# Optimization experiments

Hardware: AMD Instinct MI355X
Metric: run time of the kernel (lower is better)

The kernel has to match this reference:

```python
import jax, jax.numpy as jnp
import numpy as np

NEG_SLOPE = 0.2

def _gat_conv(x, src, dst, W, att_src, att_dst, bias, num_nodes):
    # x: [N, Fin], W: [H*C, Fin], att_*: [H, C], bias: [H*C]
    H, C = att_src.shape
    xh = (x @ W.T).reshape(num_nodes, H, C)            # [N,H,C]
    a_s = jnp.einsum('nhc,hc->nh', xh, att_src)         # [N,H]
    a_d = jnp.einsum('nhc,hc->nh', xh, att_dst)
    e = jax.nn.leaky_relu(a_s[src] + a_d[dst], NEG_SLOPE)  # [E,H]
    # segment softmax over destination node per head
    m = jax.ops.segment_max(e, dst, num_segments=num_nodes)      # [N,H]
    ex = jnp.exp(e - m[dst])
    s = jax.ops.segment_sum(ex, dst, num_segments=num_nodes)     # [N,H]
    alpha = ex / (s[dst] + 1e-16)                                # [E,H]
    msg = xh[src] * alpha[:, :, None]                            # [E,H,C]
    out = jax.ops.segment_sum(msg, dst, num_segments=num_nodes)  # [N,H,C]
    return out.reshape(num_nodes, H * C) + bias


def setup_inputs() -> dict:
    key = jax.random.key(0)
    ks = jax.random.split(key, 16)
    N, E, Fin, Hd, H1, G = 50000, 800000, 128, 128, 4, 128
    x = jax.random.normal(ks[0], (N, Fin), dtype=jnp.float32)
    edge_index = jax.random.randint(ks[1], (2, E), 0, N, dtype=jnp.int64)
    batch = jnp.sort(jax.random.randint(ks[2], (N,), 0, G, dtype=jnp.int64))
    sc1 = 1.0 / np.sqrt(Fin)
    sc2 = 1.0 / np.sqrt(Hd * H1)
    sch = 1.0 / np.sqrt(Hd)
    return {
        'x': x, 'edge_index': edge_index, 'batch': batch,
        'W1': jax.random.normal(ks[3], (Hd * H1, Fin), dtype=jnp.float32) * sc1,
        'as1': jax.random.normal(ks[4], (H1, Hd), dtype=jnp.float32) * 0.1,
        'ad1': jax.random.normal(ks[5], (H1, Hd), dtype=jnp.float32) * 0.1,
        'b1': jnp.zeros((Hd * H1,), dtype=jnp.float32),
        'W2': jax.random.normal(ks[6], (Hd, Hd * H1), dtype=jnp.float32) * sc2,
        'as2': jax.random.normal(ks[7], (1, Hd), dtype=jnp.float32) * 0.1,
        'ad2': jax.random.normal(ks[8], (1, Hd), dtype=jnp.float32) * 0.1,
        'b2': jnp.zeros((Hd,), dtype=jnp.float32),
        'Wh1': jax.random.normal(ks[9], (Hd, Hd), dtype=jnp.float32) * sch,
        'bh1': jnp.zeros((Hd,), dtype=jnp.float32),
        'Wh2': jax.random.normal(ks[10], (1, Hd), dtype=jnp.float32) * sch,
        'bh2': jnp.zeros((1,), dtype=jnp.float32),
    }


def reference(x, edge_index, batch, W1, as1, ad1, b1, W2, as2, ad2, b2, Wh1, bh1, Wh2, bh2):
    N = x.shape[0]
    G = 128  # num graphs
    # add self loops (PyG GATConv default)
    loops = jnp.arange(N, dtype=edge_index.dtype)
    src = jnp.concatenate([edge_index[0], loops])
    dst = jnp.concatenate([edge_index[1], loops])
    h = _gat_conv(x, src, dst, W1, as1, ad1, b1, N)   # [N, 512]
    h = jax.nn.elu(h)
    h = _gat_conv(h, src, dst, W2, as2, ad2, b2, N)   # [N, 128]
    h = jax.nn.elu(h)
    # global mean pool over batch
    sums = jax.ops.segment_sum(h, batch, num_segments=G)
    cnts = jax.ops.segment_sum(jnp.ones((N,), dtype=h.dtype), batch, num_segments=G)
    pooled = sums / jnp.maximum(cnts, 1.0)[:, None]   # [G, 128]
    z = jax.nn.relu(pooled @ Wh1.T + bh1)
    out = z @ Wh2.T + bh2                             # [G, 1]
    return out.reshape(-1)
```

## Files before the change

kernel.cpp:

```cpp
#include <hip/hip_runtime.h>
#include <cstdint>
#include <cstddef>

#define NEG_SLOPE 0.2f

typedef _Float16 f16x8 __attribute__((ext_vector_type(8)));
typedef _Float16 f16x2 __attribute__((ext_vector_type(2)));
typedef float    f32x4 __attribute__((ext_vector_type(4)));

__device__ __forceinline__ float leaky(float x){ return x > 0.f ? x : NEG_SLOPE * x; }
__device__ __forceinline__ float elu(float x){ return x > 0.f ? x : __expf(x) - 1.f; }

__global__ void k_wcvt(const float* __restrict__ src, _Float16* __restrict__ hi,
                       _Float16* __restrict__ lo, int n)
{
    int i = blockIdx.x * 256 + threadIdx.x;
    if (i >= n) return;
    float v = src[i];
    _Float16 h = (_Float16)v;
    hi[i] = h;
    lo[i] = (_Float16)(v - (float)h);
}

#define LSG 40
#define CP  136
template<bool FUSE_BIAS_ELU>
__global__ __launch_bounds__(256, 2) void k_gemm_h(
    const _Float16* __restrict__ A, const _Float16* __restrict__ Bh,
    const _Float16* __restrict__ Bl, const float* __restrict__ bias,
    _Float16* __restrict__ C,
    int M, int K, int lda, int ldb, int ldc,
    long aZ, long bZ, long cZ, long biasZ)
{
    __shared__ __align__(16) _Float16 smem[128 * CP];
    _Float16* As  = smem;
    _Float16* Bhs = smem + 128 * LSG;
    _Float16* Bls = smem + 256 * LSG;

    const _Float16* Ab  = A  + (size_t)blockIdx.z * aZ;
    const _Float16* Bhb = Bh + (size_t)blockIdx.z * bZ;
    const _Float16* Blb = Bl + (size_t)blockIdx.z * bZ;
    _Float16* Cb = C + (size_t)blockIdx.z * cZ;

    const int tid = threadIdx.x;
    const int wave = tid >> 6, lane = tid & 63;
    const int wm = wave >> 1, wn = wave & 1;
    const int quad = lane >> 4, l16 = lane & 15;
    const int m0 = blockIdx.x * 128;

    f32x4 acc[4][4] = {};

    for (int k0 = 0; k0 < K; k0 += 32) {
        #pragma unroll
        for (int q = 0; q < 2; ++q) {
            int idx = tid + q * 256;
            int row = idx >> 2, kq = idx & 3;
            int rg = m0 + row;
            f16x8 va = {};
            if (rg < M) va = *(const f16x8*)(Ab + (size_t)rg * lda + k0 + kq * 8);
            *(f16x8*)&As[row * LSG + kq * 8] = va;
            *(f16x8*)&Bhs[row * LSG + kq * 8] = *(const f16x8*)(Bhb + (size_t)row * ldb + k0 + kq * 8);
            *(f16x8*)&Bls[row * LSG + kq * 8] = *(const f16x8*)(Blb + (size_t)row * ldb + k0 + kq * 8);
        }
        __syncthreads();

        f16x8 af[4], bhf[4], blf[4];
        #pragma unroll
        for (int i = 0; i < 4; ++i) {
            int mr = wm * 64 + i * 16 + l16;
            af[i] = *(const f16x8*)&As[mr * LSG + quad * 8];
            int nr = wn * 64 + i * 16 + l16;
            bhf[i] = *(const f16x8*)&Bhs[nr * LSG + quad * 8];
            blf[i] = *(const f16x8*)&Bls[nr * LSG + quad * 8];
        }
        #pragma unroll
        for (int i = 0; i < 4; ++i)
            #pragma unroll
            for (int j = 0; j < 4; ++j) {
                acc[i][j] = __builtin_amdgcn_mfma_f32_16x16x32_f16(af[i], bhf[j], acc[i][j], 0, 0, 0);
                acc[i][j] = __builtin_amdgcn_mfma_f32_16x16x32_f16(af[i], blf[j], acc[i][j], 0, 0, 0);
            }
        __syncthreads();
    }

    #pragma unroll
    for (int j = 0; j < 4; ++j) {
        int n = wn * 64 + j * 16 + l16;
        float bb = 0.f;
        if (FUSE_BIAS_ELU) bb = bias[blockIdx.z * biasZ + n];
        #pragma unroll
        for (int i = 0; i < 4; ++i)
            #pragma unroll
            for (int r = 0; r < 4; ++r) {
                float v = acc[i][j][r];
                if (FUSE_BIAS_ELU) v = elu(v + bb);
                smem[(wm * 64 + i * 16 + quad * 4 + r) * CP + n] = (_Float16)v;
            }
    }
    __syncthreads();
    for (int c = tid; c < 2048; c += 256) {
        int row = c >> 4, col8 = (c & 15) * 8;
        int m = m0 + row;
        if (m < M)
            *(f16x8*)(Cb + (size_t)m * ldc + col8) = *(const f16x8*)&smem[row * CP + col8];
    }
}

__global__ __launch_bounds__(128) void k_wvec(const float* __restrict__ W1,
                                              const float* __restrict__ as1,
                                              const float* __restrict__ ad1,
                                              float* __restrict__ w_s,
                                              float* __restrict__ w_d)
{
    int h = blockIdx.x, k = threadIdx.x;
    float s = 0.f, d = 0.f;
    for (int c = 0; c < 128; ++c) {
        float w = W1[((size_t)(h * 128 + c)) * 128 + k];
        s += as1[h * 128 + c] * w;
        d += ad1[h * 128 + c] * w;
    }
    w_s[h * 128 + k] = s;
    w_d[h * 128 + k] = d;
}

__global__ __launch_bounds__(256) void k_attn_x(const float* __restrict__ x,
                                                const float* __restrict__ w_s,
                                                const float* __restrict__ w_d,
                                                float* __restrict__ a_s,
                                                float* __restrict__ a_d,
                                                _Float16* __restrict__ xh, int N)
{
    int n = blockIdx.x * 4 + (threadIdx.x >> 6);
    if (n >= N) return;
    int lane = threadIdx.x & 63;
    float2 xv = *(const float2*)(x + (size_t)n * 128 + lane * 2);
    f16x2 hv = { (_Float16)xv.x, (_Float16)xv.y };
    *(f16x2*)(xh + (size_t)n * 128 + lane * 2) = hv;
    float ps[4], pd[4];
    #pragma unroll
    for (int h = 0; h < 4; ++h) {
        float2 sv = *(const float2*)(w_s + h * 128 + lane * 2);
        float2 dv = *(const float2*)(w_d + h * 128 + lane * 2);
        ps[h] = xv.x * sv.x + xv.y * sv.y;
        pd[h] = xv.x * dv.x + xv.y * dv.y;
    }
    #pragma unroll
    for (int h = 0; h < 4; ++h)
        for (int off = 32; off; off >>= 1) {
            ps[h] += __shfl_xor(ps[h], off);
            pd[h] += __shfl_xor(pd[h], off);
        }
    if (lane == 0) {
        *(float4*)(a_s + (size_t)n * 4) = make_float4(ps[0], ps[1], ps[2], ps[3]);
        *(float4*)(a_d + (size_t)n * 4) = make_float4(pd[0], pd[1], pd[2], pd[3]);
    }
}

__global__ __launch_bounds__(256) void k_attn2(const _Float16* __restrict__ xh,
                                               const float* __restrict__ as2,
                                               const float* __restrict__ ad2,
                                               float* __restrict__ a_s,
                                               float* __restrict__ a_d, int N)
{
    int n = blockIdx.x * 4 + (threadIdx.x >> 6);
    if (n >= N) return;
    int lane = threadIdx.x & 63;
    f16x2 xv = *(const f16x2*)(xh + (size_t)n * 128 + lane * 2);
    float vx = (float)xv.x, vy = (float)xv.y;
    float2 sv = *(const float2*)(as2 + lane * 2);
    float2 dv = *(const float2*)(ad2 + lane * 2);
    float ps = vx * sv.x + vy * sv.y;
    float pd = vx * dv.x + vy * dv.y;
    for (int off = 32; off; off >>= 1) { ps += __shfl_xor(ps, off); pd += __shfl_xor(pd, off); }
    if (lane == 0) { a_s[n] = ps; a_d[n] = pd; }
}

__global__ void k_count(const int* __restrict__ ei, int* __restrict__ deg,
                        unsigned short* __restrict__ rank, int E, int Ep)
{
    int e = blockIdx.x * blockDim.x + threadIdx.x;
    if (e >= Ep) return;
    int dst = (e < E) ? ei[E + e] : (e - E);
    rank[e] = (unsigned short)atomicAdd(&deg[dst], 1);
}

__global__ __launch_bounds__(1024) void k_scanA(const int* __restrict__ deg,
                                                int* __restrict__ start,
                                                int* __restrict__ sums, int Ntot, int N)
{
    __shared__ int sm[1024];
    int tid = threadIdx.x;
    int i = blockIdx.x * 1024 + tid;
    int v = (i < N) ? deg[i] : 0;
    sm[tid] = v; __syncthreads();
    for (int off = 1; off < 1024; off <<= 1) {
        int t = (tid >= off) ? sm[tid - off] : 0;
        __syncthreads();
        sm[tid] += t;
        __syncthreads();
    }
    if (i < Ntot) start[i] = sm[tid] - v;
    if (tid == 1023) sums[blockIdx.x] = sm[1023];
}

__global__ void k_scanB(int* sums, int nb)
{
    int l = threadIdx.x;
    int v = (l < nb) ? sums[l] : 0;
    int orig = v;
    for (int off = 1; off < 64; off <<= 1) { int t = __shfl_up(v, off); if (l >= off) v += t; }
    if (l < nb) sums[l] = v - orig;
}

__global__ __launch_bounds__(1024) void k_scanC(int* __restrict__ start,
                                                const int* __restrict__ sums, int Ntot)
{
    int i = blockIdx.x * 1024 + threadIdx.x;
    if (i < Ntot) start[i] += sums[blockIdx.x];
}

__global__ void k_fill(const int* __restrict__ ei, const int* __restrict__ start,
                       const unsigned short* __restrict__ rank,
                       unsigned short* __restrict__ csr_src, int E, int Ep)
{
    int e = blockIdx.x * blockDim.x + threadIdx.x;
    if (e >= Ep) return;
    int src, dst;
    if (e < E) { src = ei[e]; dst = ei[E + e]; } else { src = dst = e - E; }
    csr_src[start[dst] + rank[e]] = (unsigned short)src;
}

__global__ __launch_bounds__(256) void k_gat1(const int* __restrict__ start,
                                              const unsigned short* __restrict__ csr,
                                              const float* __restrict__ a_s,
                                              const float* __restrict__ a_d,
                                              const _Float16* __restrict__ x,
                                              _Float16* __restrict__ agg, int N)
{
    int d = blockIdx.x * 16 + (threadIdx.x >> 4);
    if (d >= N) return;
    int g16 = threadIdx.x & 15;
    int beg = start[d], end = start[d + 1];
    int deg = end - beg;
    float4 ad4 = *(const float4*)(a_d + (size_t)d * 4);

    float sum0 = 0.f, sum1 = 0.f, sum2 = 0.f, sum3 = 0.f;
    float acc[4][8] = {};
    const _Float16* xb = x + g16 * 8;

    for (int base = 0; base < deg; base += 16) {
        int nch = deg - base; if (nch > 16) nch = 16;
        int s = 0;
        float e0 = 0.f, e1 = 0.f, e2 = 0.f, e3 = 0.f;
        if (g16 < nch) {
            s = csr[beg + base + g16];
            float4 as4 = *(const float4*)(a_s + (size_t)s * 4);
            e0 = __expf(leaky(as4.x + ad4.x));
            e1 = __expf(leaky(as4.y + ad4.y));
            e2 = __expf(leaky(as4.z + ad4.z));
            e3 = __expf(leaky(as4.w + ad4.w));
            sum0 += e0; sum1 += e1; sum2 += e2; sum3 += e3;
        }
        for (int t = 0; t < nch; ++t) {
            int   si = __shfl(s,  t, 16);
            float w0 = __shfl(e0, t, 16);
            float w1 = __shfl(e1, t, 16);
            float w2 = __shfl(e2, t, 16);
            float w3 = __shfl(e3, t, 16);
            f16x8 hv = *(const f16x8*)(xb + (size_t)si * 128);
            #pragma unroll
            for (int c = 0; c < 8; ++c) {
                float v = (float)hv[c];
                acc[0][c] += w0 * v;
                acc[1][c] += w1 * v;
                acc[2][c] += w2 * v;
                acc[3][c] += w3 * v;
            }
        }
    }
    #pragma unroll
    for (int o = 1; o < 16; o <<= 1) {
        sum0 += __shfl_xor(sum0, o, 16); sum1 += __shfl_xor(sum1, o, 16);
        sum2 += __shfl_xor(sum2, o, 16); sum3 += __shfl_xor(sum3, o, 16);
    }
    float inv[4] = { 1.f / (sum0 + 1e-16f), 1.f / (sum1 + 1e-16f),
                     1.f / (sum2 + 1e-16f), 1.f / (sum3 + 1e-16f) };
    _Float16* o = agg + (size_t)d * 512 + g16 * 8;
    #pragma unroll
    for (int h = 0; h < 4; ++h) {
        f16x8 ov;
        #pragma unroll
        for (int c = 0; c < 8; ++c) ov[c] = (_Float16)(acc[h][c] * inv[h]);
        *(f16x8*)(o + h * 128) = ov;
    }
}

__global__ __launch_bounds__(256) void k_gat2(const int* __restrict__ start,
                                              const unsigned short* __restrict__ csr,
                                              const float* __restrict__ a_s,
                                              const float* __restrict__ a_d,
                                              const _Float16* __restrict__ xh2,
                                              const float* __restrict__ b2,
                                              float* __restrict__ h2, int N)
{
    int d = blockIdx.x * 16 + (threadIdx.x >> 4);
    if (d >= N) return;
    int g16 = threadIdx.x & 15;
    int beg = start[d], end = start[d + 1];
    int deg = end - beg;
    float ad = a_d[d];

    float sum = 0.f;
    float acc[8] = {};
    const _Float16* xb = xh2 + g16 * 8;

    for (int base = 0; base < deg; base += 16) {
        int nch = deg - base; if (nch > 16) nch = 16;
        int s = 0; float e = 0.f;
        if (g16 < nch) {
            s = csr[beg + base + g16];
            e = __expf(leaky(a_s[s] + ad));
            sum += e;
        }
        for (int t = 0; t < nch; ++t) {
            int   si = __shfl(s, t, 16);
            float w  = __shfl(e, t, 16);
            f16x8 hv = *(const f16x8*)(xb + (size_t)si * 128);
            #pragma unroll
            for (int c = 0; c < 8; ++c) acc[c] += w * (float)hv[c];
        }
    }
    #pragma unroll
    for (int o = 1; o < 16; o <<= 1) sum += __shfl_xor(sum, o, 16);
    float inv = 1.f / (sum + 1e-16f);
    float ov[8];
    #pragma unroll
    for (int c = 0; c < 8; ++c) ov[c] = elu(acc[c] * inv + b2[g16 * 8 + c]);
    float* op = h2 + (size_t)d * 128 + g16 * 8;
    *(float4*)(op)     = *(float4*)&ov[0];
    *(float4*)(op + 4) = *(float4*)&ov[4];
}

__global__ void k_gbound(const int* __restrict__ batch, int* __restrict__ gstart, int N, int G)
{
    int n = blockIdx.x * blockDim.x + threadIdx.x;
    if (n >= N) return;
    int b = batch[n];
    int prev = (n == 0) ? -1 : batch[n - 1];
    for (int g = prev + 1; g <= b; ++g) gstart[g] = n;
    if (n == N - 1)
        for (int g = b + 1; g <= G; ++g) gstart[g] = N;
}

#define PCH 64
__global__ __launch_bounds__(128) void k_poolA(const float* __restrict__ h2,
                                               const int* __restrict__ batch,
                                               float* __restrict__ pooled, int N)
{
    int c = threadIdx.x;
    int n0 = blockIdx.x * PCH;
    int n1 = n0 + PCH < N ? n0 + PCH : N;
    if (n0 >= N) return;
    int g = batch[n0];
    float acc = 0.f;
    for (int n = n0; n < n1; ++n) {
        int bg = batch[n];
        if (bg != g) { atomicAdd(&pooled[(size_t)g * 128 + c], acc); acc = 0.f; g = bg; }
        acc += h2[(size_t)n * 128 + c];
    }
    atomicAdd(&pooled[(size_t)g * 128 + c], acc);
}

__global__ __launch_bounds__(128) void k_head(const float* __restrict__ pooled,
                                              const int* __restrict__ gstart,
                                              const float* __restrict__ Wh1,
                                              const float* __restrict__ bh1,
                                              const float* __restrict__ Wh2,
                                              const float* __restrict__ bh2,
                                              float* __restrict__ out)
{
    int g = blockIdx.x, c = threadIdx.x;
    __shared__ float p[128];
    __shared__ float red[128];
    float cf = (float)(gstart[g + 1] - gstart[g]); cf = cf > 1.f ? cf : 1.f;
    p[c] = pooled[(size_t)g * 128 + c] / cf;
    __syncthreads();
    float z = bh1[c];
    for (int k = 0; k < 128; ++k) z += p[k] * Wh1[c * 128 + k];
    z = z > 0.f ? z : 0.f;
    red[c] = z * Wh2[c];
    __syncthreads();
    for (int st = 64; st > 0; st >>= 1) { if (c < st) red[c] += red[c + st]; __syncthreads(); }
    if (c == 0) out[g] = red[0] + bh2[0];
}

extern "C" void kernel_launch(void* const* d_in, const int* in_sizes, int n_in,
                              void* d_out, int out_size, void* d_ws, size_t ws_size,
                              hipStream_t stream)
{
    const float* x   = (const float*)d_in[0];
    const int*   ei  = (const int*)d_in[1];
    const int*   bat = (const int*)d_in[2];
    const float* W1  = (const float*)d_in[3];
    const float* as1 = (const float*)d_in[4];
    const float* ad1 = (const float*)d_in[5];
    const float* b1  = (const float*)d_in[6];
    const float* W2  = (const float*)d_in[7];
    const float* as2 = (const float*)d_in[8];
    const float* ad2 = (const float*)d_in[9];
    const float* b2  = (const float*)d_in[10];
    const float* Wh1 = (const float*)d_in[11];
    const float* bh1 = (const float*)d_in[12];
    const float* Wh2 = (const float*)d_in[13];
    const float* bh2 = (const float*)d_in[14];
    float* out = (float*)d_out;

    const int N  = in_sizes[0] / 128;
    const int E  = in_sizes[1] / 2;
    const int Ep = E + N;
    const int G  = 128;

    char* w = (char*)d_ws;
    size_t off = 0;
    auto alloc = [&](size_t bytes) -> char* {
        char* p = w + off; off += (bytes + 511) & ~(size_t)511; return p;
    };
    _Float16* x_h  = (_Float16*)alloc((size_t)N * 128 * 2);
    _Float16* agg  = (_Float16*)alloc((size_t)N * 512 * 2);
    _Float16* h1   = (_Float16*)alloc((size_t)N * 512 * 2);
    _Float16* xh2h = (_Float16*)alloc((size_t)N * 128 * 2);
    float*    h2   = (float*)alloc((size_t)N * 128 * 4);
    float*    As1  = (float*)alloc((size_t)N * 4 * 4);
    float*    Ad1  = (float*)alloc((size_t)N * 4 * 4);
    float*    As2  = (float*)alloc((size_t)N * 4);
    float*    Ad2  = (float*)alloc((size_t)N * 4);
    float*    w_s1 = (float*)alloc(512 * 4);
    float*    w_d1 = (float*)alloc(512 * 4);
    _Float16* W1hi = (_Float16*)alloc(65536 * 2);
    _Float16* W1lo = (_Float16*)alloc(65536 * 2);
    _Float16* W2hi = (_Float16*)alloc(65536 * 2);
    _Float16* W2lo = (_Float16*)alloc(65536 * 2);
    int* startb = (int*)alloc((size_t)(N + 1) * 4);
    unsigned short* csr  = (unsigned short*)alloc((size_t)Ep * 2);
    unsigned short* rank = (unsigned short*)alloc((size_t)Ep * 2);
    int* sums   = (int*)alloc(4096);
    int* gstart = (int*)alloc((size_t)(G + 1) * 4);
    char* zbase = w + off;
    int*   deg    = (int*)alloc((size_t)N * 4);
    float* pooled = (float*)alloc((size_t)G * 128 * 4);
    size_t zbytes = (size_t)((w + off) - zbase);

    hipMemsetAsync(zbase, 0, zbytes, stream);

    k_wvec<<<4, 128, 0, stream>>>(W1, as1, ad1, w_s1, w_d1);
    k_attn_x<<<(N + 3) / 4, 256, 0, stream>>>(x, w_s1, w_d1, As1, Ad1, x_h, N);
    k_wcvt<<<256, 256, 0, stream>>>(W1, W1hi, W1lo, 65536);
    k_wcvt<<<256, 256, 0, stream>>>(W2, W2hi, W2lo, 65536);
    k_count<<<(Ep + 255) / 256, 256, 0, stream>>>(ei, deg, rank, E, Ep);
    int nb = (N + 1 + 1023) / 1024;
    k_scanA<<<nb, 1024, 0, stream>>>(deg, startb, sums, N + 1, N);
    k_scanB<<<1, 64, 0, stream>>>(sums, nb);
    k_scanC<<<nb, 1024, 0, stream>>>(startb, sums, N + 1);
    k_fill<<<(Ep + 255) / 256, 256, 0, stream>>>(ei, startb, rank, csr, E, Ep);
    k_gbound<<<(N + 255) / 256, 256, 0, stream>>>(bat, gstart, N, G);
    k_gat1<<<(N + 15) / 16, 256, 0, stream>>>(startb, csr, As1, Ad1, x_h, agg, N);
    k_gemm_h<true><<<dim3((N + 127) / 128, 1, 4), 256, 0, stream>>>(
        agg, W1hi, W1lo, b1, h1, N, 128, 512, 128, 512, 128L, 16384L, 128L, 128L);
    k_gemm_h<false><<<dim3((N + 127) / 128, 1, 1), 256, 0, stream>>>(
        h1, W2hi, W2lo, nullptr, xh2h, N, 512, 512, 512, 128, 0L, 0L, 0L, 0L);
    k_attn2<<<(N + 3) / 4, 256, 0, stream>>>(xh2h, as2, ad2, As2, Ad2, N);
    k_gat2<<<(N + 15) / 16, 256, 0, stream>>>(startb, csr, As2, Ad2, xh2h, b2, h2, N);
    k_poolA<<<(N + PCH - 1) / PCH, 128, 0, stream>>>(h2, bat, pooled, N);
    k_head<<<G, 128, 0, stream>>>(pooled, gstart, Wh1, bh1, Wh2, bh2, out);
}
```

Before: 362.2 us.

## Fuse small prep kernels, fold attn2 into GEMM epilogue, store h2 as fp16

```diff
diff --git a/kernel.cpp b/kernel.cpp
--- a/kernel.cpp
+++ b/kernel.cpp
@@ -7,28 +7,52 @@
 typedef _Float16 f16x8 __attribute__((ext_vector_type(8)));
 typedef _Float16 f16x2 __attribute__((ext_vector_type(2)));
 typedef float    f32x4 __attribute__((ext_vector_type(4)));
+typedef float    f32x2 __attribute__((ext_vector_type(2)));
 
 __device__ __forceinline__ float leaky(float x){ return x > 0.f ? x : NEG_SLOPE * x; }
 __device__ __forceinline__ float elu(float x){ return x > 0.f ? x : __expf(x) - 1.f; }
 
-__global__ void k_wcvt(const float* __restrict__ src, _Float16* __restrict__ hi,
-                       _Float16* __restrict__ lo, int n)
-{
-    int i = blockIdx.x * 256 + threadIdx.x;
-    if (i >= n) return;
-    float v = src[i];
-    _Float16 h = (_Float16)v;
-    hi[i] = h;
-    lo[i] = (_Float16)(v - (float)h);
+__global__ __launch_bounds__(256) void k_prep(const float* __restrict__ W1,
+                                              const float* __restrict__ W2,
+                                              const float* __restrict__ as1,
+                                              const float* __restrict__ ad1,
+                                              _Float16* __restrict__ W1hi, _Float16* __restrict__ W1lo,
+                                              _Float16* __restrict__ W2hi, _Float16* __restrict__ W2lo,
+                                              float* __restrict__ w_s, float* __restrict__ w_d)
+{
+    int b = blockIdx.x;
+    if (b < 512) {
+        const float* src = (b < 256) ? W1 : W2;
+        _Float16* hi = (b < 256) ? W1hi : W2hi;
+        _Float16* lo = (b < 256) ? W1lo : W2lo;
+        int i = ((b & 255) << 8) + threadIdx.x;
+        float v = src[i];
+        _Float16 h = (_Float16)v;
+        hi[i] = h;
+        lo[i] = (_Float16)(v - (float)h);
+    } else {
+        int h = (b - 512) * 2 + (threadIdx.x >> 7);
+        int k = threadIdx.x & 127;
+        float s = 0.f, d = 0.f;
+        for (int c = 0; c < 128; ++c) {
+            float w = W1[((size_t)(h * 128 + c)) * 128 + k];
+            s += as1[h * 128 + c] * w;
+            d += ad1[h * 128 + c] * w;
+        }
+        w_s[h * 128 + k] = s;
+        w_d[h * 128 + k] = d;
+    }
 }
 
 #define LSG 40
 #define CP  136
-template<bool FUSE_BIAS_ELU>
+template<bool FUSE_BIAS_ELU, bool FUSE_ATTN2>
 __global__ __launch_bounds__(256, 2) void k_gemm_h(
     const _Float16* __restrict__ A, const _Float16* __restrict__ Bh,
     const _Float16* __restrict__ Bl, const float* __restrict__ bias,
     _Float16* __restrict__ C,
+    const float* __restrict__ as2, const float* __restrict__ ad2,
+    float* __restrict__ As2, float* __restrict__ Ad2,
     int M, int K, int lda, int ldb, int ldc,
     long aZ, long bZ, long cZ, long biasZ)
 {
@@ -104,23 +128,26 @@
         if (m < M)
             *(f16x8*)(Cb + (size_t)m * ldc + col8) = *(const f16x8*)&smem[row * CP + col8];
     }
-}
-
-__global__ __launch_bounds__(128) void k_wvec(const float* __restrict__ W1,
-                                              const float* __restrict__ as1,
-                                              const float* __restrict__ ad1,
-                                              float* __restrict__ w_s,
-                                              float* __restrict__ w_d)
-{
-    int h = blockIdx.x, k = threadIdx.x;
-    float s = 0.f, d = 0.f;
-    for (int c = 0; c < 128; ++c) {
-        float w = W1[((size_t)(h * 128 + c)) * 128 + k];
-        s += as1[h * 128 + c] * w;
-        d += ad1[h * 128 + c] * w;
-    }
-    w_s[h * 128 + k] = s;
-    w_d[h * 128 + k] = d;
+    if (FUSE_ATTN2) {
+        int row = tid >> 1, half = tid & 1;
+        int d = m0 + row;
+        float ss = 0.f, sd = 0.f;
+        const _Float16* rp = &smem[row * CP + half * 64];
+        #pragma unroll
+        for (int c8 = 0; c8 < 8; ++c8) {
+            f16x8 v = *(const f16x8*)(rp + c8 * 8);
+            #pragma unroll
+            for (int c = 0; c < 8; ++c) {
+                float f = (float)v[c];
+                int n = half * 64 + c8 * 8 + c;
+                ss += f * as2[n];
+                sd += f * ad2[n];
+            }
+        }
+        ss += __shfl_xor(ss, 1);
+        sd += __shfl_xor(sd, 1);
+        if (half == 0 && d < M) { As2[d] = ss; Ad2[d] = sd; }
+    }
 }
 
 __global__ __launch_bounds__(256) void k_attn_x(const float* __restrict__ x,
@@ -156,32 +183,25 @@
     }
 }
 
-__global__ __launch_bounds__(256) void k_attn2(const _Float16* __restrict__ xh,
-                                               const float* __restrict__ as2,
-                                               const float* __restrict__ ad2,
-                                               float* __restrict__ a_s,
-                                               float* __restrict__ a_d, int N)
-{
-    int n = blockIdx.x * 4 + (threadIdx.x >> 6);
-    if (n >= N) return;
-    int lane = threadIdx.x & 63;
-    f16x2 xv = *(const f16x2*)(xh + (size_t)n * 128 + lane * 2);
-    float vx = (float)xv.x, vy = (float)xv.y;
-    float2 sv = *(const float2*)(as2 + lane * 2);
-    float2 dv = *(const float2*)(ad2 + lane * 2);
-    float ps = vx * sv.x + vy * sv.y;
-    float pd = vx * dv.x + vy * dv.y;
-    for (int off = 32; off; off >>= 1) { ps += __shfl_xor(ps, off); pd += __shfl_xor(pd, off); }
-    if (lane == 0) { a_s[n] = ps; a_d[n] = pd; }
-}
-
 __global__ void k_count(const int* __restrict__ ei, int* __restrict__ deg,
-                        unsigned short* __restrict__ rank, int E, int Ep)
-{
-    int e = blockIdx.x * blockDim.x + threadIdx.x;
-    if (e >= Ep) return;
-    int dst = (e < E) ? ei[E + e] : (e - E);
-    rank[e] = (unsigned short)atomicAdd(&deg[dst], 1);
+                        unsigned short* __restrict__ rank,
+                        const int* __restrict__ batch, int* __restrict__ gstart,
+                        int E, int Ep, int N, int G, int nbc)
+{
+    if ((int)blockIdx.x < nbc) {
+        int e = blockIdx.x * 256 + threadIdx.x;
+        if (e >= Ep) return;
+        int dst = (e < E) ? ei[E + e] : (e - E);
+        rank[e] = (unsigned short)atomicAdd(&deg[dst], 1);
+    } else {
+        int n = (blockIdx.x - nbc) * 256 + threadIdx.x;
+        if (n >= N) return;
+        int b = batch[n];
+        int prev = (n == 0) ? -1 : batch[n - 1];
+        for (int g = prev + 1; g <= b; ++g) gstart[g] = n;
+        if (n == N - 1)
+            for (int g = b + 1; g <= G; ++g) gstart[g] = N;
+    }
 }
 
 __global__ __launch_bounds__(1024) void k_scanA(const int* __restrict__ deg,
@@ -245,7 +265,7 @@
     float4 ad4 = *(const float4*)(a_d + (size_t)d * 4);
 
     float sum0 = 0.f, sum1 = 0.f, sum2 = 0.f, sum3 = 0.f;
-    float acc[4][8] = {};
+    f32x2 acc[4][4] = {};
     const _Float16* xb = x + g16 * 8;
 
     for (int base = 0; base < deg; base += 16) {
@@ -268,14 +288,14 @@
             float w2 = __shfl(e2, t, 16);
             float w3 = __shfl(e3, t, 16);
             f16x8 hv = *(const f16x8*)(xb + (size_t)si * 128);
-            #pragma unroll
-            for (int c = 0; c < 8; ++c) {
-                float v = (float)hv[c];
-                acc[0][c] += w0 * v;
-                acc[1][c] += w1 * v;
-                acc[2][c] += w2 * v;
-                acc[3][c] += w3 * v;
-            }
+            f32x2 v0 = { (float)hv[0], (float)hv[1] };
+            f32x2 v1 = { (float)hv[2], (float)hv[3] };
+            f32x2 v2 = { (float)hv[4], (float)hv[5] };
+            f32x2 v3 = { (float)hv[6], (float)hv[7] };
+            acc[0][0] += w0 * v0; acc[0][1] += w0 * v1; acc[0][2] += w0 * v2; acc[0][3] += w0 * v3;
+            acc[1][0] += w1 * v0; acc[1][1] += w1 * v1; acc[1][2] += w1 * v2; acc[1][3] += w1 * v3;
+            acc[2][0] += w2 * v0; acc[2][1] += w2 * v1; acc[2][2] += w2 * v2; acc[2][3] += w2 * v3;
+            acc[3][0] += w3 * v0; acc[3][1] += w3 * v1; acc[3][2] += w3 * v2; acc[3][3] += w3 * v3;
         }
     }
     #pragma unroll
@@ -290,7 +310,10 @@
     for (int h = 0; h < 4; ++h) {
         f16x8 ov;
         #pragma unroll
-        for (int c = 0; c < 8; ++c) ov[c] = (_Float16)(acc[h][c] * inv[h]);
+        for (int p = 0; p < 4; ++p) {
+            ov[2 * p]     = (_Float16)(acc[h][p].x * inv[h]);
+            ov[2 * p + 1] = (_Float16)(acc[h][p].y * inv[h]);
+        }
         *(f16x8*)(o + h * 128) = ov;
     }
 }
@@ -301,7 +324,7 @@
                                               const float* __restrict__ a_d,
                                               const _Float16* __restrict__ xh2,
                                               const float* __restrict__ b2,
-                                              float* __restrict__ h2, int N)
+                                              _Float16* __restrict__ h2, int N)
 {
     int d = blockIdx.x * 16 + (threadIdx.x >> 4);
     if (d >= N) return;
@@ -311,7 +334,7 @@
     float ad = a_d[d];
 
     float sum = 0.f;
-    float acc[8] = {};
+    f32x2 acc[4] = {};
     const _Float16* xb = xh2 + g16 * 8;
 
     for (int base = 0; base < deg; base += 16) {
@@ -326,34 +349,27 @@
             int   si = __shfl(s, t, 16);
             float w  = __shfl(e, t, 16);
             f16x8 hv = *(const f16x8*)(xb + (size_t)si * 128);
-            #pragma unroll
-            for (int c = 0; c < 8; ++c) acc[c] += w * (float)hv[c];
+            f32x2 v0 = { (float)hv[0], (float)hv[1] };
+            f32x2 v1 = { (float)hv[2], (float)hv[3] };
+            f32x2 v2 = { (float)hv[4], (float)hv[5] };
+            f32x2 v3 = { (float)hv[6], (float)hv[7] };
+            acc[0] += w * v0; acc[1] += w * v1; acc[2] += w * v2; acc[3] += w * v3;
         }
     }
     #pragma unroll
     for (int o = 1; o < 16; o <<= 1) sum += __shfl_xor(sum, o, 16);
     float inv = 1.f / (sum + 1e-16f);
-    float ov[8];
-    #pragma unroll
-    for (int c = 0; c < 8; ++c) ov[c] = elu(acc[c] * inv + b2[g16 * 8 + c]);
-    float* op = h2 + (size_t)d * 128 + g16 * 8;
-    *(float4*)(op)     = *(float4*)&ov[0];
-    *(float4*)(op + 4) = *(float4*)&ov[4];
-}
-
-__global__ void k_gbound(const int* __restrict__ batch, int* __restrict__ gstart, int N, int G)
-{
-    int n = blockIdx.x * blockDim.x + threadIdx.x;
-    if (n >= N) return;
-    int b = batch[n];
-    int prev = (n == 0) ? -1 : batch[n - 1];
-    for (int g = prev + 1; g <= b; ++g) gstart[g] = n;
-    if (n == N - 1)
-        for (int g = b + 1; g <= G; ++g) gstart[g] = N;
+    f16x8 ov;
+    #pragma unroll
+    for (int p = 0; p < 4; ++p) {
+        ov[2 * p]     = (_Float16)elu(acc[p].x * inv + b2[g16 * 8 + 2 * p]);
+        ov[2 * p + 1] = (_Float16)elu(acc[p].y * inv + b2[g16 * 8 + 2 * p + 1]);
+    }
+    *(f16x8*)(h2 + (size_t)d * 128 + g16 * 8) = ov;
 }
 
 #define PCH 64
-__global__ __launch_bounds__(128) void k_poolA(const float* __restrict__ h2,
+__global__ __launch_bounds__(128) void k_poolA(const _Float16* __restrict__ h2,
                                                const int* __restrict__ batch,
                                                float* __restrict__ pooled, int N)
 {
@@ -366,7 +382,7 @@
     for (int n = n0; n < n1; ++n) {
         int bg = batch[n];
         if (bg != g) { atomicAdd(&pooled[(size_t)g * 128 + c], acc); acc = 0.f; g = bg; }
-        acc += h2[(size_t)n * 128 + c];
+        acc += (float)h2[(size_t)n * 128 + c];
     }
     atomicAdd(&pooled[(size_t)g * 128 + c], acc);
 }
@@ -429,7 +445,7 @@
     _Float16* agg  = (_Float16*)alloc((size_t)N * 512 * 2);
     _Float16* h1   = (_Float16*)alloc((size_t)N * 512 * 2);
     _Float16* xh2h = (_Float16*)alloc((size_t)N * 128 * 2);
-    float*    h2   = (float*)alloc((size_t)N * 128 * 4);
+    _Float16* h2   = (_Float16*)alloc((size_t)N * 128 * 2);
     float*    As1  = (float*)alloc((size_t)N * 4 * 4);
     float*    Ad1  = (float*)alloc((size_t)N * 4 * 4);
     float*    As2  = (float*)alloc((size_t)N * 4);
@@ -452,23 +468,22 @@
 
     hipMemsetAsync(zbase, 0, zbytes, stream);
 
-    k_wvec<<<4, 128, 0, stream>>>(W1, as1, ad1, w_s1, w_d1);
+    k_prep<<<514, 256, 0, stream>>>(W1, W2, as1, ad1, W1hi, W1lo, W2hi, W2lo, w_s1, w_d1);
     k_attn_x<<<(N + 3) / 4, 256, 0, stream>>>(x, w_s1, w_d1, As1, Ad1, x_h, N);
-    k_wcvt<<<256, 256, 0, stream>>>(W1, W1hi, W1lo, 65536);
-    k_wcvt<<<256, 256, 0, stream>>>(W2, W2hi, W2lo, 65536);
-    k_count<<<(Ep + 255) / 256, 256, 0, stream>>>(ei, deg, rank, E, Ep);
+    int nbc = (Ep + 255) / 256, nbg = (N + 255) / 256;
+    k_count<<<nbc + nbg, 256, 0, stream>>>(ei, deg, rank, bat, gstart, E, Ep, N, G, nbc);
     int nb = (N + 1 + 1023) / 1024;
     k_scanA<<<nb, 1024, 0, stream>>>(deg, startb, sums, N + 1, N);
     k_scanB<<<1, 64, 0, stream>>>(sums, nb);
     k_scanC<<<nb, 1024, 0, stream>>>(startb, sums, N + 1);
     k_fill<<<(Ep + 255) / 256, 256, 0, stream>>>(ei, startb, rank, csr, E, Ep);
-    k_gbound<<<(N + 255) / 256, 256, 0, stream>>>(bat, gstart, N, G);
     k_gat1<<<(N + 15) / 16, 256, 0, stream>>>(startb, csr, As1, Ad1, x_h, agg, N);
-    k_gemm_h<true><<<dim3((N + 127) / 128, 1, 4), 256, 0, stream>>>(
-        agg, W1hi, W1lo, b1, h1, N, 128, 512, 128, 512, 128L, 16384L, 128L, 128L);
-    k_gemm_h<false><<<dim3((N + 127) / 128, 1, 1), 256, 0, stream>>>(
-        h1, W2hi, W2lo, nullptr, xh2h, N, 512, 512, 512, 128, 0L, 0L, 0L, 0L);
-    k_attn2<<<(N + 3) / 4, 256, 0, stream>>>(xh2h, as2, ad2, As2, Ad2, N);
+    k_gemm_h<true, false><<<dim3((N + 127) / 128, 1, 4), 256, 0, stream>>>(
+        agg, W1hi, W1lo, b1, h1, nullptr, nullptr, nullptr, nullptr,
+        N, 128, 512, 128, 512, 128L, 16384L, 128L, 128L);
+    k_gemm_h<false, true><<<dim3((N + 127) / 128, 1, 1), 256, 0, stream>>>(
+        h1, W2hi, W2lo, nullptr, xh2h, as2, ad2, As2, Ad2,
+        N, 512, 512, 512, 128, 0L, 0L, 0L, 0L);
     k_gat2<<<(N + 15) / 16, 256, 0, stream>>>(startb, csr, As2, Ad2, xh2h, b2, h2, N);
     k_poolA<<<(N + PCH - 1) / PCH, 128, 0, stream>>>(h2, bat, pooled, N);
     k_head<<<G, 128, 0, stream>>>(pooled, gstart, Wh1, bh1, Wh2, bh2, out);
```

Result: faster. 352.1 us (-2.8%).
